# Kernel tuning notes

Measured on AMD Instinct MI355X. Metric: run time of the kernel, lower is better.

## Reference

```python
import jax, jax.numpy as jnp
import numpy as np

C = 256  # inplanes == planes
EPS = 1e-5


def _cb(p):
    # per-channel param -> broadcastable NCHW
    return p[None, :, None, None]


def binary_act(x):
    # forward: sign(x); backward: piecewise-polynomial STE
    poly = jnp.where(x < -1.0, -1.0,
           jnp.where(x < 0.0, x * x + 2.0 * x,
           jnp.where(x < 1.0, -x * x + 2.0 * x, 1.0)))
    return jax.lax.stop_gradient(jnp.sign(x) - poly) + poly


def bin_weight(w):
    # forward: per-out-channel mean(|w|) * sign(w); backward: through clamp(w,-1,1)
    scale = jax.lax.stop_gradient(jnp.mean(jnp.abs(w), axis=(1, 2, 3), keepdims=True))
    cl = jnp.clip(w, -1.0, 1.0)
    return jax.lax.stop_gradient(scale * jnp.sign(w) - cl) + cl


def conv(x, w, pad):
    return jax.lax.conv_general_dilated(
        x, w, window_strides=(1, 1), padding=((pad, pad), (pad, pad)),
        dimension_numbers=('NCHW', 'OIHW', 'NCHW'))


def bn(x, g, b, m, v):
    inv = g * jax.lax.rsqrt(v + EPS)
    return x * _cb(inv) + _cb(b - m * inv)


def prelu(x, a):
    return jnp.where(x > 0, x, _cb(a) * x)


def setup_inputs() -> dict:
    key = jax.random.key(0)
    ks = jax.random.split(key, 3)
    z = jnp.zeros((C,), jnp.float32)
    o = jnp.ones((C,), jnp.float32)
    return {
        'x':  jax.random.normal(ks[0], (32, C, 56, 56), jnp.float32),
        'w3': jax.random.uniform(ks[1], (C, C, 3, 3), jnp.float32) * 0.001,
        'w1': jax.random.uniform(ks[2], (C, C, 1, 1), jnp.float32) * 0.001,
        'b11': z, 'b12': z, 'b13': z, 'b21': z, 'b22': z, 'b23': z,
        'g1': o, 'be1': z, 'm1': z, 'v1': o,
        'g2': o, 'be2': z, 'm2': z, 'v2': o,
        'a1': jnp.full((C,), 0.25, jnp.float32),
        'a2': jnp.full((C,), 0.25, jnp.float32),
    }


def reference(x, w3, w1, b11, b12, b13, b21, b22, b23,
              g1, be1, m1, v1, g2, be2, m2, v2, a1, a2):
    # branch 1: bias -> binarize -> binary 3x3 conv -> BN -> residual
    out1 = binary_act(x + _cb(b11))
    out1 = conv(out1, bin_weight(w3), pad=1)
    out1 = bn(out1, g1, be1, m1, v1)
    out1 = x + out1
    out1 = prelu(out1 + _cb(b12), a1) + _cb(b13)
    # branch 2: bias -> binarize -> binary 1x1 conv -> BN -> residual
    out2 = binary_act(out1 + _cb(b21))
    out2 = conv(out2, bin_weight(w1), pad=0)
    out2 = bn(out2, g2, be2, m2, v2) + out1
    out2 = prelu(out2 + _cb(b22), a2) + _cb(b23)
    return out2
```

## Files before the change

### kernel.cpp

```cpp
#include <hip/hip_runtime.h>
#include <hip/hip_bf16.h>


#define CCH  256
#define PIMG 3136
#define SPIX 3364
#define WPAD 58

typedef __attribute__((ext_vector_type(4))) int intx4;

#define GLOAD16(gp, lp) __builtin_amdgcn_global_load_lds( \
    (const __attribute__((address_space(1))) unsigned int*)(gp), \
    (__attribute__((address_space(3))) unsigned int*)(lp), 16, 0, 0)

__device__ __forceinline__ signed char sgnc(float v) {
    return (v > 0.f) ? 1 : ((v < 0.f) ? -1 : 0);
}

__global__ void transpose_sign(const float* __restrict__ x,
                               const float* __restrict__ b11,
                               signed char* __restrict__ spad) {
    const int hp  = blockIdx.x;
    const int cbg = blockIdx.y;
    const int n   = blockIdx.z;
    const int t   = threadIdx.x;
    __shared__ __align__(16) signed char tile[128 * 60];

    const size_t obase = ((size_t)cbg * 32 + n) * SPIX + (size_t)hp * WPAD;

    if (hp == 0 || hp == 57) {
        for (int it = 0; it < 8; ++it) {
            int lin = t + it * 256;
            if (lin >= 1856) break;
            int wp = lin >> 5;
            int c4 = (lin & 31) * 4;
            *(int*)(spad + (obase + wp) * 128 + c4) = 0;
        }
        return;
    }

    const int h = hp - 1;
    for (int it = 0; it < 7; ++it) {
        int lin  = t + it * 256;
        int c    = lin / 14;
        int col4 = lin - c * 14;
        int cg   = cbg * 128 + c;
        const float4 xv = *(const float4*)(x +
            ((size_t)(n * CCH + cg)) * PIMG + h * 56 + col4 * 4);
        float bb = b11[cg];
        int w = (sgnc(xv.x + bb) & 0xff)
              | ((sgnc(xv.y + bb) & 0xff) << 8)
              | ((sgnc(xv.z + bb) & 0xff) << 16)
              | ((sgnc(xv.w + bb) & 0xff) << 24);
        *(int*)(&tile[c * 60 + col4 * 4]) = w;
    }
    __syncthreads();

    for (int it = 0; it < 2; ++it) {
        int task = t + it * 256;
        if (task >= 480) break;
        int g  = task >> 5;
        int c4 = task & 31;
        unsigned int w[4];
        #pragma unroll
        for (int cc = 0; cc < 4; ++cc) {
            const signed char* rowp = &tile[(c4 * 4 + cc) * 60];
            unsigned int A = (g == 0)  ? 0u : *(const unsigned int*)(rowp + (g - 1) * 4);
            unsigned int B = (g < 14)  ? *(const unsigned int*)(rowp + g * 4) : 0u;
            w[cc] = (A >> 24) | (B << 8);
        }
        unsigned int p01_0 = __builtin_amdgcn_perm(w[1], w[0], 0x05010400u);
        unsigned int p01_1 = __builtin_amdgcn_perm(w[1], w[0], 0x07030602u);
        unsigned int p23_0 = __builtin_amdgcn_perm(w[3], w[2], 0x05010400u);
        unsigned int p23_1 = __builtin_amdgcn_perm(w[3], w[2], 0x07030602u);
        unsigned int o0 = __builtin_amdgcn_perm(p23_0, p01_0, 0x05040100u);
        unsigned int o1 = __builtin_amdgcn_perm(p23_0, p01_0, 0x07060302u);
        unsigned int o2 = __builtin_amdgcn_perm(p23_1, p01_1, 0x05040100u);
        unsigned int o3 = __builtin_amdgcn_perm(p23_1, p01_1, 0x07060302u);
        unsigned int ov[4] = {o0, o1, o2, o3};
        #pragma unroll
        for (int p = 0; p < 4; ++p) {
            int wp = 4 * g + p;
            if (wp < 58)
                *(int*)(spad + (obase + wp) * 128 + c4 * 4) = (int)ov[p];
        }
    }
}

__global__ void prep_w(const float* __restrict__ w3, const float* __restrict__ w1,
                       const float* __restrict__ g1, const float* __restrict__ be1,
                       const float* __restrict__ m1, const float* __restrict__ v1,
                       const float* __restrict__ g2, const float* __restrict__ be2,
                       const float* __restrict__ m2, const float* __restrict__ v2,
                       signed char* __restrict__ wq3f, signed char* __restrict__ wq1f,
                       float* __restrict__ k2s, float* __restrict__ k2b,
                       float* __restrict__ k3s, float* __restrict__ k3b) {
    const int o = blockIdx.x;
    const int t = threadIdx.x;
    __shared__ float red[256];
    if (o < 256) {
        const float* wp = w3 + (size_t)o * 2304;
        float s = 0.f;
        for (int i = t; i < 2304; i += 256) s += fabsf(wp[i]);
        red[t] = s; __syncthreads();
        for (int k = 128; k > 0; k >>= 1) { if (t < k) red[t] += red[t + k]; __syncthreads(); }
        float scale = red[0] * (1.0f / 2304.0f);
        for (int i = t; i < 2304; i += 256) {
            int c = i / 9; int r9 = i - c * 9;
            int cbg = c >> 7, cl = c & 127;
            int ks = cl >> 6, qd = (cl >> 4) & 3, b = cl & 15;
            wq3f[(size_t)(((r9 * 2 + cbg) * 2 + ks)) * 16384 +
                 (o >> 4) * 1024 + qd * 256 + (o & 15) * 16 + b] = sgnc(wp[i]);
        }
        if (t == 0) {
            float inv = g1[o] * rsqrtf(v1[o] + 1e-5f);
            k2s[o] = scale * inv;
            k2b[o] = be1[o] - m1[o] * inv;
        }
    } else {
        const int o1 = o - 256;
        float w = w1[(size_t)o1 * 256 + t];
        red[t] = fabsf(w); __syncthreads();
        for (int k = 128; k > 0; k >>= 1) { if (t < k) red[t] += red[t + k]; __syncthreads(); }
        float scale = red[0] * (1.0f / 256.0f);
        int cbg = t >> 7, cl = t & 127;
        int ks = cl >> 6, qd = (cl >> 4) & 3, b = cl & 15;
        wq1f[(size_t)((cbg * 2 + ks)) * 16384 +
             (o1 >> 4) * 1024 + qd * 256 + (o1 & 15) * 16 + b] = sgnc(w);
        if (t == 0) {
            float inv = g2[o1] * rsqrtf(v2[o1] + 1e-5f);
            k3s[o1] = scale * inv;
            k3b[o1] = be2[o1] - m2[o1] * inv;
        }
    }
}


#define LOADB(ph, bf) { \
    const int cbg_ = (ph) / 18, rem_ = (ph) % 18, r9_ = rem_ >> 1, ks_ = rem_ & 1; \
    const signed char* bp_ = wq3f + \
        (size_t)((((r9_ * 2 + cbg_) * 2 + ks_) * 16 + wid * 4) * 1024) + lane * 16; \
    _Pragma("unroll") \
    for (int j_ = 0; j_ < 4; ++j_) bf[j_] = *(const intx4*)(bp_ + j_ * 1024); }

#define LOADA(ph, af) { \
    const int cbg_ = (ph) / 18, rem_ = (ph) % 18, r9_ = rem_ >> 1, ks_ = rem_ & 1; \
    const int shift_ = (r9_ / 3) * WPAD + (r9_ % 3); \
    _Pragma("unroll") \
    for (int i_ = 0; i_ < 4; ++i_) { \
        const int r_  = prow[i_] + shift_; \
        const int gg_ = (ks_ * 4 + quad) ^ (r_ & 7); \
        af[i_] = *(const intx4*)(&As[cbg_][r_ * 128 + gg_ * 16]); \
    } }

#define MFMAP(af, bf) { \
    __builtin_amdgcn_s_setprio(1); \
    _Pragma("unroll") \
    for (int i_ = 0; i_ < 4; ++i_) \
        _Pragma("unroll") \
        for (int j_ = 0; j_ < 4; ++j_) \
            acc[i_][j_] = __builtin_amdgcn_mfma_i32_16x16x64_i8( \
                af[i_], bf[j_], acc[i_][j_], 0, 0, 0); \
    __builtin_amdgcn_s_setprio(0); }

__global__ __launch_bounds__(256, 2) void gemm_fused(
    const signed char* __restrict__ spad, const signed char* __restrict__ wq3f,
    const signed char* __restrict__ wq1f, const float* __restrict__ x,
    const float* __restrict__ k2s, const float* __restrict__ k2b,
    const float* __restrict__ k3s, const float* __restrict__ k3b,
    const float* __restrict__ b12, const float* __restrict__ b13,
    const float* __restrict__ b21, const float* __restrict__ a1,
    const float* __restrict__ b22, const float* __restrict__ b23,
    const float* __restrict__ a2, float* __restrict__ out) {
    __shared__ __align__(16) signed char As[2][192 * 128];
    const int t    = threadIdx.x;
    const int tile = blockIdx.x;
    const int n    = blockIdx.y;
    const int lane = t & 63;
    const int wid  = t >> 6;
    const int quad = lane >> 4;
    const int l16  = lane & 15;

    const int p0t    = tile * 64;
    const int h0     = p0t / 56;
    const int w0     = p0t - h0 * 56;
    const int pstart = h0 * WPAD + w0;

    int prow[4];
    #pragma unroll
    for (int i = 0; i < 4; ++i) {
        int p = p0t + i * 16 + l16;
        int h = p / 56, w = p - h * 56;
        prow[i] = h * WPAD + w - pstart;
    }

    const int rbase = wid * 8 + (lane >> 3);
    const int gsw   = (lane & 7) ^ (rbase & 7);

    for (int cbg = 0; cbg < 2; ++cbg) {
        const size_t cbase = ((size_t)(cbg * 32 + n)) * SPIX + pstart;
        #pragma unroll
        for (int k = 0; k < 6; ++k) {
            const int row = k * 32 + rbase;
            const signed char* gp = spad + (cbase + row) * 128 + gsw * 16;
            GLOAD16(gp, &As[cbg][(k * 4 + wid) * 1024]);
        }
    }
    __syncthreads();

    intx4 acc[4][4] = {};
    {
        intx4 bfS[4][4], afS[2][4];
        LOADB(0, bfS[0])
        LOADB(1, bfS[1])
        LOADB(2, bfS[2])
        LOADA(0, afS[0])
        #pragma unroll
        for (int ph = 0; ph < 36; ++ph) {
            if (ph + 1 < 36) LOADA(ph + 1, afS[(ph + 1) & 1])
            if (ph + 3 < 36) LOADB(ph + 3, bfS[(ph + 3) & 3])
            MFMAP(afS[ph & 1], bfS[ph & 3])
        }
    }

    __syncthreads();

    signed char* sgnL = &As[0][0];

    float out1r[4][4][4];
    #pragma unroll
    for (int j = 0; j < 4; ++j) {
        const int o = wid * 64 + j * 16 + l16;
        const float sc = k2s[o], bt = k2b[o];
        const float v12 = b12[o], v13 = b13[o], v21 = b21[o], va = a1[o];
        #pragma unroll
        for (int i = 0; i < 4; ++i) {
            const int p0 = p0t + i * 16 + quad * 4;
            const float4 xv = *(const float4*)(x + ((size_t)(n * CCH + o)) * PIMG + p0);
            float rr[4] = {xv.x, xv.y, xv.z, xv.w};
            #pragma unroll
            for (int r = 0; r < 4; ++r) {
                float v  = (float)acc[i][j][r] * sc + bt + rr[r];
                float tt = v + v12;
                float o1 = ((tt > 0.f) ? tt : va * tt) + v13;
                out1r[i][j][r] = o1;
                const int pl = i * 16 + quad * 4 + r;
                sgnL[pl * 256 + (((wid * 4 + j) ^ (pl & 15)) << 4) + l16] =
                    sgnc(o1 + v21);
            }
        }
    }
    __syncthreads();

    intx4 acc2[4][4] = {};
    #pragma unroll
    for (int ph = 0; ph < 4; ++ph) {
        const int cbg2 = ph >> 1, ks2 = ph & 1;
        intx4 af2[4], bf2[4];
        const signed char* bp = wq1f +
            (size_t)(((cbg2 * 2 + ks2) * 16 + wid * 4) * 1024) + lane * 16;
        #pragma unroll
        for (int j = 0; j < 4; ++j) bf2[j] = *(const intx4*)(bp + j * 1024);
        const int q16 = cbg2 * 8 + ks2 * 4 + quad;
        #pragma unroll
        for (int i = 0; i < 4; ++i) {
            const int m = i * 16 + l16;
            af2[i] = *(const intx4*)(&sgnL[m * 256 + ((q16 ^ (m & 15)) << 4)]);
        }
        #pragma unroll
        for (int i = 0; i < 4; ++i)
            #pragma unroll
            for (int j = 0; j < 4; ++j)
                acc2[i][j] = __builtin_amdgcn_mfma_i32_16x16x64_i8(
                    af2[i], bf2[j], acc2[i][j], 0, 0, 0);
    }

    #pragma unroll
    for (int j = 0; j < 4; ++j) {
        const int o = wid * 64 + j * 16 + l16;
        const float sc = k3s[o], bt = k3b[o];
        const float v22 = b22[o], v23 = b23[o], va = a2[o];
        #pragma unroll
        for (int i = 0; i < 4; ++i) {
            const int p0 = p0t + i * 16 + quad * 4;
            float res[4];
            #pragma unroll
            for (int r = 0; r < 4; ++r) {
                float v  = (float)acc2[i][j][r] * sc + bt + out1r[i][j][r];
                float tt = v + v22;
                res[r] = ((tt > 0.f) ? tt : va * tt) + v23;
            }
            float4 ov; ov.x = res[0]; ov.y = res[1]; ov.z = res[2]; ov.w = res[3];
            *(float4*)(out + ((size_t)(n * CCH + o)) * PIMG + p0) = ov;
        }
    }
}

extern "C" void kernel_launch(void* const* d_in, const int* in_sizes, int n_in,
                              void* d_out, int out_size, void* d_ws, size_t ws_size,
                              hipStream_t stream) {
    const float* x   = (const float*)d_in[0];
    const float* w3  = (const float*)d_in[1];
    const float* w1  = (const float*)d_in[2];
    const float* b11 = (const float*)d_in[3];
    const float* b12 = (const float*)d_in[4];
    const float* b13 = (const float*)d_in[5];
    const float* b21 = (const float*)d_in[6];
    const float* b22 = (const float*)d_in[7];
    const float* b23 = (const float*)d_in[8];
    const float* g1  = (const float*)d_in[9];
    const float* be1 = (const float*)d_in[10];
    const float* m1  = (const float*)d_in[11];
    const float* v1  = (const float*)d_in[12];
    const float* g2  = (const float*)d_in[13];
    const float* be2 = (const float*)d_in[14];
    const float* m2  = (const float*)d_in[15];
    const float* v2  = (const float*)d_in[16];
    const float* a1  = (const float*)d_in[17];
    const float* a2  = (const float*)d_in[18];
    float* out = (float*)d_out;

    char* ws = (char*)d_ws;
    signed char* spad = (signed char*)(ws);
    signed char* wq3f = (signed char*)(ws + 27816192);
    signed char* wq1f = (signed char*)(ws + 28406016);
    float* k2s = (float*)(ws + 28471552);
    float* k2b = k2s + 256;
    float* k3s = k2s + 512;
    float* k3b = k2s + 768;

    transpose_sign<<<dim3(58, 2, 32), 256, 0, stream>>>(x, b11, spad);
    prep_w<<<512, 256, 0, stream>>>(w3, w1, g1, be1, m1, v1, g2, be2, m2, v2,
                                    wq3f, wq1f, k2s, k2b, k3s, k3b);
    gemm_fused<<<dim3(49, 32), 256, 0, stream>>>(spad, wq3f, wq1f, x,
                                                 k2s, k2b, k3s, k3b,
                                                 b12, b13, b21, a1,
                                                 b22, b23, a2, out);
}
```

Measured before the change: 302.6 us.

## Cut register pressure to fit three blocks per CU in fused GEMM

The 3x3 conv main loop drops its 4-deep B and 2-deep A register prefetch rings for a simple two-buffer ping-pong that loads A and B together one phase ahead. The 1x1 conv stage is split into two halves over output-column groups, so only half the second accumulator array is live at once. Launch bounds rise from 2 to 3 blocks per multiprocessor. The goal is higher occupancy to hide latency, at the cost of a shallower prefetch distance for global weight loads, which may expose more load latency.

```diff
diff --git a/kernel.cpp b/kernel.cpp
--- a/kernel.cpp
+++ b/kernel.cpp
@@ -136,16 +136,13 @@
 }
 
 
-#define LOADB(ph, bf) { \
+#define LOADP(ph, af, bf) { \
     const int cbg_ = (ph) / 18, rem_ = (ph) % 18, r9_ = rem_ >> 1, ks_ = rem_ & 1; \
+    const int shift_ = (r9_ / 3) * WPAD + (r9_ % 3); \
     const signed char* bp_ = wq3f + \
         (size_t)((((r9_ * 2 + cbg_) * 2 + ks_) * 16 + wid * 4) * 1024) + lane * 16; \
     _Pragma("unroll") \
-    for (int j_ = 0; j_ < 4; ++j_) bf[j_] = *(const intx4*)(bp_ + j_ * 1024); }
-
-#define LOADA(ph, af) { \
-    const int cbg_ = (ph) / 18, rem_ = (ph) % 18, r9_ = rem_ >> 1, ks_ = rem_ & 1; \
-    const int shift_ = (r9_ / 3) * WPAD + (r9_ % 3); \
+    for (int j_ = 0; j_ < 4; ++j_) bf[j_] = *(const intx4*)(bp_ + j_ * 1024); \
     _Pragma("unroll") \
     for (int i_ = 0; i_ < 4; ++i_) { \
         const int r_  = prow[i_] + shift_; \
@@ -163,7 +160,7 @@
                 af[i_], bf[j_], acc[i_][j_], 0, 0, 0); \
     __builtin_amdgcn_s_setprio(0); }
 
-__global__ __launch_bounds__(256, 2) void gemm_fused(
+__global__ __launch_bounds__(256, 3) void gemm_fused(
     const signed char* __restrict__ spad, const signed char* __restrict__ wq3f,
     const signed char* __restrict__ wq1f, const float* __restrict__ x,
     const float* __restrict__ k2s, const float* __restrict__ k2b,
@@ -210,16 +207,14 @@
 
     intx4 acc[4][4] = {};
     {
-        intx4 bfS[4][4], afS[2][4];
-        LOADB(0, bfS[0])
-        LOADB(1, bfS[1])
-        LOADB(2, bfS[2])
-        LOADA(0, afS[0])
-        #pragma unroll
-        for (int ph = 0; ph < 36; ++ph) {
-            if (ph + 1 < 36) LOADA(ph + 1, afS[(ph + 1) & 1])
-            if (ph + 3 < 36) LOADB(ph + 3, bfS[(ph + 3) & 3])
-            MFMAP(afS[ph & 1], bfS[ph & 3])
+        intx4 afA[4], bfA[4], afB[4], bfB[4];
+        LOADP(0, afA, bfA)
+        #pragma unroll
+        for (int ph = 0; ph < 36; ph += 2) {
+            if (ph + 1 < 36) LOADP(ph + 1, afB, bfB)
+            MFMAP(afA, bfA)
+            if (ph + 2 < 36) LOADP(ph + 2, afA, bfA)
+            if (ph + 1 < 36) MFMAP(afB, bfB)
         }
     }
 
@@ -252,46 +247,51 @@
     }
     __syncthreads();
 
-    intx4 acc2[4][4] = {};
     #pragma unroll
-    for (int ph = 0; ph < 4; ++ph) {
-        const int cbg2 = ph >> 1, ks2 = ph & 1;
-        intx4 af2[4], bf2[4];
-        const signed char* bp = wq1f +
-            (size_t)(((cbg2 * 2 + ks2) * 16 + wid * 4) * 1024) + lane * 16;
-        #pragma unroll
-        for (int j = 0; j < 4; ++j) bf2[j] = *(const intx4*)(bp + j * 1024);
-        const int q16 = cbg2 * 8 + ks2 * 4 + quad;
-        #pragma unroll
-        for (int i = 0; i < 4; ++i) {
-            const int m = i * 16 + l16;
-            af2[i] = *(const intx4*)(&sgnL[m * 256 + ((q16 ^ (m & 15)) << 4)]);
-        }
-        #pragma unroll
-        for (int i = 0; i < 4; ++i)
-            #pragma unroll
-            for (int j = 0; j < 4; ++j)
-                acc2[i][j] = __builtin_amdgcn_mfma_i32_16x16x64_i8(
-                    af2[i], bf2[j], acc2[i][j], 0, 0, 0);
-    }
-
-    #pragma unroll
-    for (int j = 0; j < 4; ++j) {
-        const int o = wid * 64 + j * 16 + l16;
-        const float sc = k3s[o], bt = k3b[o];
-        const float v22 = b22[o], v23 = b23[o], va = a2[o];
-        #pragma unroll
-        for (int i = 0; i < 4; ++i) {
-            const int p0 = p0t + i * 16 + quad * 4;
-            float res[4];
-            #pragma unroll
-            for (int r = 0; r < 4; ++r) {
-                float v  = (float)acc2[i][j][r] * sc + bt + out1r[i][j][r];
-                float tt = v + v22;
-                res[r] = ((tt > 0.f) ? tt : va * tt) + v23;
+    for (int jh = 0; jh < 2; ++jh) {
+        intx4 acc2[4][2] = {};
+        #pragma unroll
+        for (int ph = 0; ph < 4; ++ph) {
+            const int cbg2 = ph >> 1, ks2 = ph & 1;
+            intx4 af2[4], bf2[2];
+            const signed char* bp = wq1f +
+                (size_t)(((cbg2 * 2 + ks2) * 16 + wid * 4) * 1024) + lane * 16;
+            #pragma unroll
+            for (int jj = 0; jj < 2; ++jj)
+                bf2[jj] = *(const intx4*)(bp + (jh * 2 + jj) * 1024);
+            const int q16 = cbg2 * 8 + ks2 * 4 + quad;
+            #pragma unroll
+            for (int i = 0; i < 4; ++i) {
+                const int m = i * 16 + l16;
+                af2[i] = *(const intx4*)(&sgnL[m * 256 + ((q16 ^ (m & 15)) << 4)]);
             }
-            float4 ov; ov.x = res[0]; ov.y = res[1]; ov.z = res[2]; ov.w = res[3];
-            *(float4*)(out + ((size_t)(n * CCH + o)) * PIMG + p0) = ov;
+            #pragma unroll
+            for (int i = 0; i < 4; ++i)
+                #pragma unroll
+                for (int jj = 0; jj < 2; ++jj)
+                    acc2[i][jj] = __builtin_amdgcn_mfma_i32_16x16x64_i8(
+                        af2[i], bf2[jj], acc2[i][jj], 0, 0, 0);
+        }
+
+        #pragma unroll
+        for (int jj = 0; jj < 2; ++jj) {
+            const int j = jh * 2 + jj;
+            const int o = wid * 64 + j * 16 + l16;
+            const float sc = k3s[o], bt = k3b[o];
+            const float v22 = b22[o], v23 = b23[o], va = a2[o];
+            #pragma unroll
+            for (int i = 0; i < 4; ++i) {
+                const int p0 = p0t + i * 16 + quad * 4;
+                float res[4];
+                #pragma unroll
+                for (int r = 0; r < 4; ++r) {
+                    float v  = (float)acc2[i][jj][r] * sc + bt + out1r[i][j][r];
+                    float tt = v + v22;
+                    res[r] = ((tt > 0.f) ? tt : va * tt) + v23;
+                }
+                float4 ov; ov.x = res[0]; ov.y = res[1]; ov.z = res[2]; ov.w = res[3];
+                *(float4*)(out + ((size_t)(n * CCH + o)) * PIMG + p0) = ov;
+            }
         }
     }
 }
```

New measurement: 332.9 us. 10.0% more time.
